# Kernel optimization log

Measured on AMD Instinct MI355X. Metric: run time of the kernel, lower is better.

## Reference

```python
import jax, jax.numpy as jnp
import numpy as np

SIZE = 256


def setup_inputs() -> dict:
    key = jax.random.key(0)
    ks = jax.random.split(key, 16)
    B, T, S, V = 16, 128, 512, 32000
    s = SIZE
    inp = {}
    inp["inputs"] = jax.random.randint(ks[0], (B, T), 0, V)
    inp["features"] = jax.random.normal(ks[1], (B, S, 2 * s), dtype=jnp.float32)
    # parameters (PyTorch-style: y = x @ W.T + b)
    inp["emb"] = jax.random.normal(ks[2], (V, s), dtype=jnp.float32)
    inp["W_ih"] = jax.random.normal(ks[3], (4 * s, 2 * s), dtype=jnp.float32) * 0.05
    inp["W_hh"] = jax.random.normal(ks[4], (4 * s, s), dtype=jnp.float32) * 0.05
    inp["b_ih"] = jax.random.normal(ks[5], (4 * s,), dtype=jnp.float32) * 0.05
    inp["b_hh"] = jax.random.normal(ks[6], (4 * s,), dtype=jnp.float32) * 0.05
    inp["Wq"] = jax.random.normal(ks[7], (s, s), dtype=jnp.float32) * 0.05
    inp["bq"] = jax.random.normal(ks[8], (s,), dtype=jnp.float32) * 0.05
    inp["Wk"] = jax.random.normal(ks[9], (s, 2 * s), dtype=jnp.float32) * 0.05
    inp["bk"] = jax.random.normal(ks[10], (s,), dtype=jnp.float32) * 0.05
    inp["Wv"] = jax.random.normal(ks[11], (s, 2 * s), dtype=jnp.float32) * 0.05
    inp["bv"] = jax.random.normal(ks[12], (s,), dtype=jnp.float32) * 0.05
    inp["Wo"] = jax.random.normal(ks[13], (V, 2 * s), dtype=jnp.float32) * 0.05
    inp["bo"] = jax.random.normal(ks[14], (V,), dtype=jnp.float32) * 0.05
    return inp


def _decode(inputs, features, emb, W_ih, W_hh, b_ih, b_hh,
            Wq, bq, Wk, bk, Wv, bv, Wo, bo):
    B, T = inputs.shape
    s = emb.shape[1]
    embeddings = emb[inputs]                      # [B, T, s]
    # features are constant across timesteps -> hoist key/value projections
    keys = features @ Wk.T + bk                   # [B, S, s]
    values = features @ Wv.T + bv                 # [B, S, s]

    def step(carry, emb_t):
        h, c, context = carry
        x = jnp.concatenate([emb_t, context], axis=1)          # [B, 2s]
        gates = x @ W_ih.T + b_ih + h @ W_hh.T + b_hh          # [B, 4s]
        i, f, g, o = jnp.split(gates, 4, axis=1)               # PyTorch gate order
        i, f, o = jax.nn.sigmoid(i), jax.nn.sigmoid(f), jax.nn.sigmoid(o)
        g = jnp.tanh(g)
        c_new = f * c + i * g
        h_new = o * jnp.tanh(c_new)
        # attention
        query = h_new @ Wq.T + bq                              # [B, s]
        scores = jnp.einsum('bsd,bd->bs', keys, query)         # [B, S]
        weights = jax.nn.softmax(scores, axis=1)
        ctx = jnp.einsum('bsd,bs->bd', values, weights)        # [B, s]
        out = jnp.concatenate([h_new, ctx], axis=1) @ Wo.T + bo  # [B, V]
        return (h_new, c_new, ctx), out

    h0 = jnp.zeros((B, s), dtype=embeddings.dtype)
    c0 = jnp.zeros((B, s), dtype=embeddings.dtype)
    ctx0 = jnp.zeros((B, s), dtype=embeddings.dtype)
    _, outs = jax.lax.scan(step, (h0, c0, ctx0), jnp.swapaxes(embeddings, 0, 1))
    return jnp.swapaxes(outs, 0, 1)               # [B, T, V]


def reference(inputs, features, emb, W_ih, W_hh, b_ih, b_hh,
              Wq, bq, Wk, bk, Wv, bv, Wo, bo):
    return _decode(inputs, features, emb, W_ih, W_hh, b_ih, b_hh,
                   Wq, bq, Wk, bk, Wv, bv, Wo, bo)
```

## Files before the change

kernel.cpp:

```cpp
#include <hip/hip_runtime.h>
#include <hip/hip_fp16.h>

#define DEVI __device__ __forceinline__

typedef __attribute__((ext_vector_type(4))) float f32x4;
typedef __attribute__((ext_vector_type(8))) short bf16x8;
typedef __attribute__((ext_vector_type(8))) _Float16 f16x8;
typedef __attribute__((ext_vector_type(2))) _Float16 f16x2;
typedef unsigned long long ull;

DEVI ushort f2bf(float x) {
  union { float f; unsigned u; } v; v.f = x;
  unsigned r = v.u + 0x7fffu + ((v.u >> 16) & 1u);
  return (ushort)(r >> 16);
}
DEVI float bf2f(ushort b) {
  union { unsigned u; float f; } v; v.u = ((unsigned)b) << 16; return v.f;
}
DEVI unsigned packh2(float a, float b) {
  return ((unsigned)__half_as_ushort(__float2half(b)) << 16) |
         (unsigned)__half_as_ushort(__float2half(a));
}
DEVI float dot2(unsigned a, unsigned b, float c) {
#if __has_builtin(__builtin_amdgcn_fdot2)
  return __builtin_amdgcn_fdot2(__builtin_bit_cast(f16x2, a),
                                __builtin_bit_cast(f16x2, b), c, false);
#else
  f16x2 ha = __builtin_bit_cast(f16x2, a), hb = __builtin_bit_cast(f16x2, b);
  return c + (float)ha[0] * (float)hb[0] + (float)ha[1] * (float)hb[1];
#endif
}
DEVI float sigmoidf_(float x) { return 1.f / (1.f + __expf(-x)); }
DEVI float tanh_fast(float x) {
  float e = __expf(2.f * x);
  return 1.f - 2.f / (e + 1.f);
}

DEVI void gstore64(ull* p, ull v) {
  __hip_atomic_store(p, v, __ATOMIC_RELAXED, __HIP_MEMORY_SCOPE_AGENT);
}
DEVI ull gload64(const ull* p) {
  return __hip_atomic_load(p, __ATOMIC_RELAXED, __HIP_MEMORY_SCOPE_AGENT);
}

template<bool SPLIT, bool ABF16, bool BBF16, bool SWZ>
__global__ __launch_bounds__(256)
void gemm_kernel(const void* __restrict__ A_, int lda, const int* __restrict__ Aidx,
                 const void* __restrict__ Bw_, int ldb,
                 const float* __restrict__ bias, float* __restrict__ C,
                 int N, int K)
{
  constexpr int BK  = SPLIT ? 32 : 64;
  constexpr int LDT = BK + 8;
  constexpr int NV  = (128 * BK / 4) / 256;

  __shared__ ushort Ah[128 * LDT];
  __shared__ ushort Bh[128 * LDT];
  __shared__ ushort Al[SPLIT ? 128 * LDT : 4];
  __shared__ ushort Bl[SPLIT ? 128 * LDT : 4];

  int bm, bn;
  if (SWZ) {
    int bid = blockIdx.x;
    int r8 = bid & 7, k = bid >> 3;
    int x = k & 15, yhi = k >> 4;
    int y = yhi * 8 + r8;
    if (y >= 250) return;
    bm = x * 128; bn = y * 128;
  } else {
    bm = blockIdx.x * 128; bn = blockIdx.y * 128;
  }

  const int tid  = threadIdx.x;
  const int lane = tid & 63, wave = tid >> 6;
  const int wr   = wave >> 1, wc = wave & 1;
  const int fr   = lane & 15, quad = lane >> 4;

  f32x4 acc[4][4] = {};

  for (int kt = 0; kt < K; kt += BK) {
    __syncthreads();
#pragma unroll
    for (int i = 0; i < NV; ++i) {
      int v   = i * 256 + tid;
      int row = v / (BK / 4);
      int c4  = (v % (BK / 4)) * 4;
      int arow = Aidx ? Aidx[bm + row] : (bm + row);
      if (ABF16) {
        const ushort* A = (const ushort*)A_;
        ushort4 h = *reinterpret_cast<const ushort4*>(A + (size_t)arow * lda + kt + c4);
        *reinterpret_cast<ushort4*>(&Ah[row * LDT + c4]) = h;
      } else {
        const float* A = (const float*)A_;
        const float4 x = *reinterpret_cast<const float4*>(A + (size_t)arow * lda + kt + c4);
        ushort4 h; h.x = f2bf(x.x); h.y = f2bf(x.y); h.z = f2bf(x.z); h.w = f2bf(x.w);
        *reinterpret_cast<ushort4*>(&Ah[row * LDT + c4]) = h;
        if (SPLIT) {
          ushort4 l;
          l.x = f2bf(x.x - bf2f(h.x)); l.y = f2bf(x.y - bf2f(h.y));
          l.z = f2bf(x.z - bf2f(h.z)); l.w = f2bf(x.w - bf2f(h.w));
          *reinterpret_cast<ushort4*>(&Al[row * LDT + c4]) = l;
        }
      }
    }
#pragma unroll
    for (int i = 0; i < NV; ++i) {
      int v   = i * 256 + tid;
      int row = v / (BK / 4);
      int c4  = (v % (BK / 4)) * 4;
      if (BBF16) {
        const ushort* B16 = (const ushort*)Bw_;
        ushort4 h = *reinterpret_cast<const ushort4*>(B16 + (size_t)(bn + row) * ldb + kt + c4);
        *reinterpret_cast<ushort4*>(&Bh[row * LDT + c4]) = h;
      } else {
        const float* Bw = (const float*)Bw_;
        const float4 x = *reinterpret_cast<const float4*>(Bw + (size_t)(bn + row) * ldb + kt + c4);
        ushort4 h; h.x = f2bf(x.x); h.y = f2bf(x.y); h.z = f2bf(x.z); h.w = f2bf(x.w);
        *reinterpret_cast<ushort4*>(&Bh[row * LDT + c4]) = h;
        if (SPLIT) {
          ushort4 l;
          l.x = f2bf(x.x - bf2f(h.x)); l.y = f2bf(x.y - bf2f(h.y));
          l.z = f2bf(x.z - bf2f(h.z)); l.w = f2bf(x.w - bf2f(h.w));
          *reinterpret_cast<ushort4*>(&Bl[row * LDT + c4]) = l;
        }
      }
    }
    __syncthreads();
#pragma unroll
    for (int ks = 0; ks < BK; ks += 32) {
      bf16x8 ah[4], bh[4];
#pragma unroll
      for (int i = 0; i < 4; ++i) {
        ah[i] = *reinterpret_cast<const bf16x8*>(&Ah[(wr * 64 + i * 16 + fr) * LDT + ks + quad * 8]);
        bh[i] = *reinterpret_cast<const bf16x8*>(&Bh[(wc * 64 + i * 16 + fr) * LDT + ks + quad * 8]);
      }
      if (SPLIT) {
        bf16x8 al[4], bl[4];
#pragma unroll
        for (int i = 0; i < 4; ++i) {
          al[i] = *reinterpret_cast<const bf16x8*>(&Al[(wr * 64 + i * 16 + fr) * LDT + ks + quad * 8]);
          bl[i] = *reinterpret_cast<const bf16x8*>(&Bl[(wc * 64 + i * 16 + fr) * LDT + ks + quad * 8]);
        }
#pragma unroll
        for (int i = 0; i < 4; ++i)
#pragma unroll
          for (int j = 0; j < 4; ++j) {
            acc[i][j] = __builtin_amdgcn_mfma_f32_16x16x32_bf16(ah[i], bh[j], acc[i][j], 0, 0, 0);
            acc[i][j] = __builtin_amdgcn_mfma_f32_16x16x32_bf16(ah[i], bl[j], acc[i][j], 0, 0, 0);
            acc[i][j] = __builtin_amdgcn_mfma_f32_16x16x32_bf16(al[i], bh[j], acc[i][j], 0, 0, 0);
          }
      } else {
#pragma unroll
        for (int i = 0; i < 4; ++i)
#pragma unroll
          for (int j = 0; j < 4; ++j)
            acc[i][j] = __builtin_amdgcn_mfma_f32_16x16x32_bf16(ah[i], bh[j], acc[i][j], 0, 0, 0);
      }
    }
  }
#pragma unroll
  for (int i = 0; i < 4; ++i)
#pragma unroll
    for (int j = 0; j < 4; ++j)
#pragma unroll
      for (int r = 0; r < 4; ++r) {
        int m = bm + wr * 64 + i * 16 + quad * 4 + r;
        int n = bn + wc * 64 + j * 16 + fr;
        float vv = acc[i][j][r];
        if (bias) vv += bias[n];
        C[(size_t)m * N + n] = vv;
      }
}

__global__ __launch_bounds__(256)
void prep2_kernel(const float* __restrict__ Wk, const float* __restrict__ Wq,
                  const float* __restrict__ Wv, const float* __restrict__ bk,
                  const float* __restrict__ bq, const float* __restrict__ b_ih,
                  const float* __restrict__ b_hh, const float* __restrict__ bv,
                  float* __restrict__ Bcomb, float* __restrict__ bias512,
                  float* __restrict__ bsum, float* __restrict__ wkbq,
                  float* __restrict__ cbbv)
{
  __shared__ float col[256];
  __shared__ float red[256];
  const int blk = blockIdx.x, tid = threadIdx.x;
  if (blk < 256) {
    const int e = blk;
    float cv = Wq[(size_t)tid * 256 + e];
    col[tid] = cv;
    red[tid] = bk[tid] * cv;
    __syncthreads();
    float a0 = 0.f, a1 = 0.f;
    for (int d = 0; d < 256; ++d) {
      float wq = col[d];
      a0 = fmaf(Wk[(size_t)d * 512 + tid], wq, a0);
      a1 = fmaf(Wk[(size_t)d * 512 + 256 + tid], wq, a1);
    }
    Bcomb[(size_t)(256 + e) * 512 + tid] = a0;
    Bcomb[(size_t)(256 + e) * 512 + 256 + tid] = a1;
    if (tid == 0) {
      float s = 0.f;
      for (int d = 0; d < 256; ++d) s += red[d];
      bias512[256 + e] = s;
    }
  } else {
    for (int i = tid; i < 256 * 512 / 4; i += 256)
      reinterpret_cast<float4*>(Bcomb)[i] = reinterpret_cast<const float4*>(Wv)[i];
    bias512[tid] = bv[tid];
    for (int i = tid; i < 1024; i += 256) bsum[i] = b_ih[i] + b_hh[i];
    float bqv = bq[tid];
    col[tid] = bqv;
    red[tid] = bk[tid] * bqv;
    __syncthreads();
    float a0 = 0.f, a1 = 0.f;
    for (int d = 0; d < 256; ++d) {
      float v = col[d];
      a0 = fmaf(Wk[(size_t)d * 512 + tid], v, a0);
      a1 = fmaf(Wk[(size_t)d * 512 + 256 + tid], v, a1);
    }
    wkbq[tid] = a0; wkbq[256 + tid] = a1;
    if (tid == 0) {
      float s = 0.f;
      for (int d = 0; d < 256; ++d) s += red[d];
      cbbv[0] = s;
    }
  }
}

__global__ void sb2_kernel(const float* __restrict__ features,
                           const float* __restrict__ wkbq,
                           const float* __restrict__ cbbv,
                           float* __restrict__ sb)
{
  int row  = blockIdx.x * 4 + (threadIdx.x >> 6);
  int lane = threadIdx.x & 63;
  const float* fr = features + (size_t)row * 512;
  float acc = 0.f;
#pragma unroll
  for (int k = 0; k < 8; ++k) acc = fmaf(fr[k * 64 + lane], wkbq[k * 64 + lane], acc);
#pragma unroll
  for (int off = 1; off < 64; off <<= 1) acc += __shfl_xor(acc, off);
  if (lane == 0) sb[row] = acc + cbbv[0];
}

__global__ void cvt_kernel(const float* __restrict__ src, ushort* __restrict__ dst, int n4)
{
  int i = blockIdx.x * 256 + threadIdx.x;
  if (i < n4) {
    float4 x = reinterpret_cast<const float4*>(src)[i];
    ushort4 h; h.x = f2bf(x.x); h.y = f2bf(x.y); h.z = f2bf(x.z); h.w = f2bf(x.w);
    reinterpret_cast<ushort4*>(dst)[i] = h;
  }
}

struct ScanSmem2 {
  unsigned k2p[64][131];
  unsigned vtp[256][35];
  unsigned xw[288];
  unsigned psp[32];
  float Erow[128];
  float gout[128];
  float ml[8][2];
  float part[8][130];
  float sc[8][64];
  float sbs[64];
};

DEVI int xwi(int w) { return (w >> 6) * 72 + (w & 63); }

__global__ __launch_bounds__(512, 1)
void scan2_kernel(const float* __restrict__ E, const float* __restrict__ KV2,
                  const float* __restrict__ sbg,
                  const float* __restrict__ W_ih, const float* __restrict__ W_hh,
                  ushort* __restrict__ hcb16,
                  ull* __restrict__ Hx,
                  ull* __restrict__ Px)
{
  extern __shared__ char smraw[];
  ScanSmem2& sm = *reinterpret_cast<ScanSmem2*>(smraw);
  const int g = blockIdx.x, tid = threadIdx.x;
  const int b = g >> 3, ss = g & 7;

  for (int idx = tid; idx < 64 * 128; idx += 512) {
    int j = idx >> 7, i = idx & 127;
    const float* src = KV2 + (size_t)(b * 512 + ss * 64 + j) * 512 + 256 + 2 * i;
    sm.k2p[j][i] = packh2(src[0], src[1]);
  }
  for (int idx = tid; idx < 256 * 32; idx += 512) {
    int e = idx >> 5, jp = idx & 31;
    float v0 = KV2[(size_t)(b * 512 + ss * 64 + 2 * jp) * 512 + e];
    float v1 = KV2[(size_t)(b * 512 + ss * 64 + 2 * jp + 1) * 512 + e];
    sm.vtp[e][jp] = packh2(v0, v1);
  }
  if (tid < 64) sm.sbs[tid] = sbg[b * 512 + ss * 64 + tid];
  for (int i = tid; i < 288; i += 512) sm.xw[i] = 0;

  const int r  = tid >> 2, h4 = tid & 3;
  const int grow = (r >> 5) * 256 + ss * 32 + (r & 31);
  const float* wsrc = (h4 < 2)
      ? (W_ih + (size_t)grow * 512 + 256 + h4 * 128)
      : (W_hh + (size_t)grow * 256 + (h4 - 2) * 128);
  unsigned wreg[64];
#pragma unroll
  for (int i = 0; i < 32; ++i) {
    float4 w4 = reinterpret_cast<const float4*>(wsrc)[i];
    wreg[2 * i]     = packh2(w4.x, w4.y);
    wreg[2 * i + 1] = packh2(w4.z, w4.w);
  }

  float c_reg = 0.f;
  __syncthreads();

  const size_t hxb = (size_t)b * 128;
  const size_t pxb = (size_t)b * (8 * 130);

  for (int t = 0; t <= 128; ++t) {
    float epf = 0.f;
    if (t < 128 && tid < 128)
      epf = E[(size_t)(b * 128 + t) * 1024 + (tid >> 5) * 256 + ss * 32 + (tid & 31)];

    float accg = 0.f;
    if (t > 0) {
      const unsigned tag = (unsigned)t;
      const ull* PxP = Px + (size_t)((t - 1) & 1) * (16 * 8 * 130) + pxb;
      const int e2 = tid & 127, q = tid >> 7;
      const ull* p1 = &PxP[(2 * q) * 130 + e2];
      const ull* p2 = &PxP[(2 * q + 1) * 130 + e2];
      ull w1 = gload64(p1), w2 = gload64(p2);
      const ull* pm = &PxP[(tid >> 1) * 130 + 128 + (tid & 1)];
      ull wm = (tid < 16) ? gload64(pm) : 0;

      if (h4 >= 2) {
        const unsigned* xsrc = sm.xw + h4 * 72;
#pragma unroll
        for (int i = 0; i < 16; ++i) {
          uint4 xv = *reinterpret_cast<const uint4*>(xsrc + 4 * i);
          accg = dot2(wreg[4 * i + 0], xv.x, accg);
          accg = dot2(wreg[4 * i + 1], xv.y, accg);
          accg = dot2(wreg[4 * i + 2], xv.z, accg);
          accg = dot2(wreg[4 * i + 3], xv.w, accg);
        }
      }

      if (tid < 16) {
        while ((unsigned)(wm >> 32) != tag) { __builtin_amdgcn_s_sleep(1); wm = gload64(pm); }
        sm.ml[tid >> 1][tid & 1] = __uint_as_float((unsigned)wm);
      }
      while ((unsigned)(w1 >> 32) != tag) { __builtin_amdgcn_s_sleep(1); w1 = gload64(p1); }
      while ((unsigned)(w2 >> 32) != tag) { __builtin_amdgcn_s_sleep(1); w2 = gload64(p2); }
      __syncthreads();
      float M = sm.ml[0][0];
#pragma unroll
      for (int s3 = 1; s3 < 8; ++s3) M = fmaxf(M, sm.ml[s3][0]);
      float L = 0.f;
#pragma unroll
      for (int s3 = 0; s3 < 8; ++s3) L += sm.ml[s3][1] * __expf(sm.ml[s3][0] - M);
      float rcpL = 1.f / L;
      float wf0 = __expf(sm.ml[2 * q][0] - M);
      float wf1 = __expf(sm.ml[2 * q + 1][0] - M);
      f16x2 x1 = __builtin_bit_cast(f16x2, (unsigned)w1);
      f16x2 x2 = __builtin_bit_cast(f16x2, (unsigned)w2);
      float2 pw0; pw0.x = wf0 * (float)x1[0] + wf1 * (float)x2[0];
      float2 pw1; pw1.x = wf0 * (float)x1[1] + wf1 * (float)x2[1];
      sm.part[2 * q][e2]     = pw0.x;
      sm.part[2 * q + 1][e2] = pw1.x;
      __syncthreads();
      {
        const int l = tid & 63;
        float2 f0[8];
#pragma unroll
        for (int s4 = 0; s4 < 8; ++s4)
          f0[s4] = *reinterpret_cast<const float2*>(&sm.part[s4][2 * l]);
        float c00 = (f0[0].x + f0[2].x + f0[4].x + f0[6].x) * rcpL;
        float c01 = (f0[1].x + f0[3].x + f0[5].x + f0[7].x) * rcpL;
        float c10 = (f0[0].y + f0[2].y + f0[4].y + f0[6].y) * rcpL;
        float c11 = (f0[1].y + f0[3].y + f0[5].y + f0[7].y) * rcpL;
        sm.xw[xwi(2 * l)]     = packh2(c00, c01);
        sm.xw[xwi(2 * l + 1)] = packh2(c10, c11);
        if (tid < 64) {
          ushort4 st;
          st.x = f2bf(c00); st.y = f2bf(c01); st.z = f2bf(c10); st.w = f2bf(c11);
          *reinterpret_cast<ushort4*>(
              hcb16 + (size_t)(b * 128 + (t - 1)) * 512 + 256 + 4 * l) = st;
        }
      }
    }
    if (t == 128) break;
    if (tid < 128) sm.Erow[tid] = epf;

    if (t > 0) {
      asm volatile("s_waitcnt lgkmcnt(0)" ::: "memory");
      __builtin_amdgcn_sched_barrier(0);
      if (h4 < 2) {
        const unsigned* xsrc = sm.xw + h4 * 72;
#pragma unroll
        for (int i = 0; i < 16; ++i) {
          uint4 xv = *reinterpret_cast<const uint4*>(xsrc + 4 * i);
          accg = dot2(wreg[4 * i + 0], xv.x, accg);
          accg = dot2(wreg[4 * i + 1], xv.y, accg);
          accg = dot2(wreg[4 * i + 2], xv.z, accg);
          accg = dot2(wreg[4 * i + 3], xv.w, accg);
        }
      }
    }
    accg += __shfl_xor(accg, 1);
    accg += __shfl_xor(accg, 2);
    if (h4 == 0) sm.gout[r] = accg;
    __syncthreads();

    if (tid < 32) {
      float gi = sm.gout[tid]      + sm.Erow[tid];
      float gf = sm.gout[32 + tid] + sm.Erow[32 + tid];
      float gg = sm.gout[64 + tid] + sm.Erow[64 + tid];
      float go = sm.gout[96 + tid] + sm.Erow[96 + tid];
      float iv = sigmoidf_(gi), fv = sigmoidf_(gf), ov = sigmoidf_(go);
      float gv = tanh_fast(gg);
      c_reg = fv * c_reg + iv * gv;
      float hn = ov * tanh_fast(c_reg);
      hcb16[(size_t)(b * 128 + t) * 512 + ss * 32 + tid] = f2bf(hn);
      float ho = __shfl_xor(hn, 1);
      if (!(tid & 1)) {
        unsigned pk = packh2(hn, ho);
        int w = ss * 16 + (tid >> 1);
        sm.xw[xwi(128 + w)] = pk;
        gstore64(&Hx[(size_t)(t & 1) * 2048 + hxb + w],
                 ((ull)(unsigned)(t + 1) << 32) | pk);
      }
    }
    if (tid < 128 && (tid >> 4) != ss) {
      const ull* hp = &Hx[(size_t)(t & 1) * 2048 + hxb + tid];
      ull w = gload64(hp);
      while ((unsigned)(w >> 32) != (unsigned)(t + 1)) {
        __builtin_amdgcn_s_sleep(1); w = gload64(hp);
      }
      sm.xw[xwi(128 + tid)] = (unsigned)w;
    }
    __syncthreads();

    {
      const int j = tid & 63, qq = tid >> 6;
      float acc2 = 0.f;
#pragma unroll
      for (int i = 0; i < 16; ++i)
        acc2 = dot2(sm.k2p[j][qq * 16 + i], sm.xw[xwi(128 + qq * 16 + i)], acc2);
      sm.sc[qq][j] = acc2;
    }
    __syncthreads();
    if (tid < 64) {
      float s = sm.sc[0][tid] + sm.sc[1][tid] + sm.sc[2][tid] + sm.sc[3][tid]
              + sm.sc[4][tid] + sm.sc[5][tid] + sm.sc[6][tid] + sm.sc[7][tid]
              + sm.sbs[tid];
      float mx = s;
#pragma unroll
      for (int off = 1; off < 64; off <<= 1) mx = fmaxf(mx, __shfl_xor(mx, off));
      float p = __expf(s - mx);
      float ls = p;
#pragma unroll
      for (int off = 1; off < 64; off <<= 1) ls += __shfl_xor(ls, off);
      if (tid == 0) {
        ull tg = (ull)(unsigned)(t + 1) << 32;
        ull* PxS = Px + (size_t)(t & 1) * (16 * 8 * 130) + pxb + ss * 130;
        gstore64(&PxS[128], tg | __float_as_uint(mx));
        gstore64(&PxS[129], tg | __float_as_uint(ls));
      }
      float ph = __shfl_xor(p, 1);
      if (!(tid & 1)) sm.psp[tid >> 1] = packh2(p, ph);
    }
    __syncthreads();
    if (tid < 256) {
      float acc2 = 0.f;
#pragma unroll
      for (int jp = 0; jp < 32; ++jp) acc2 = dot2(sm.psp[jp], sm.vtp[tid][jp], acc2);
      float ao = __shfl_xor(acc2, 1);
      if (!(tid & 1)) {
        ull* PxS = Px + (size_t)(t & 1) * (16 * 8 * 130) + pxb + ss * 130;
        gstore64(&PxS[tid >> 1], ((ull)(unsigned)(t + 1) << 32) | packh2(acc2, ao));
      }
    }
  }
}

extern "C" void kernel_launch(void* const* d_in, const int* in_sizes, int n_in,
                              void* d_out, int out_size, void* d_ws, size_t ws_size,
                              hipStream_t stream)
{
  const int*   inputs   = (const int*)  d_in[0];
  const float* features = (const float*)d_in[1];
  const float* emb      = (const float*)d_in[2];
  const float* W_ih     = (const float*)d_in[3];
  const float* W_hh     = (const float*)d_in[4];
  const float* b_ih     = (const float*)d_in[5];
  const float* b_hh     = (const float*)d_in[6];
  const float* Wq       = (const float*)d_in[7];
  const float* bq       = (const float*)d_in[8];
  const float* Wk       = (const float*)d_in[9];
  const float* bk       = (const float*)d_in[10];
  const float* Wv       = (const float*)d_in[11];
  const float* bv       = (const float*)d_in[12];
  const float* Wo       = (const float*)d_in[13];
  const float* bo       = (const float*)d_in[14];
  float* out = (float*)d_out;

  char* ws = (char*)d_ws;
  size_t off = 0;
  auto alloc = [&](size_t bytes) -> char* {
    char* p = ws + off;
    off += (bytes + 255) & ~size_t(255);
    return p;
  };
  float*  KV2   = (float*) alloc((size_t)8192 * 512 * 4);
  float*  E     = (float*) alloc((size_t)2048 * 1024 * 4);
  float*  Bcomb = (float*) alloc((size_t)512 * 512 * 4);
  float*  bias512 = (float*)alloc((size_t)512 * 4);
  float*  sb    = (float*) alloc((size_t)8192 * 4);
  float*  bsum  = (float*) alloc((size_t)1024 * 4);
  float*  wkbq  = (float*) alloc((size_t)512 * 4);
  float*  cbbv  = (float*) alloc((size_t)64 * 4);
  ushort* hcb16 = (ushort*)alloc((size_t)2048 * 512 * 2);
  ull*    Hx    = (ull*)   alloc((size_t)2 * 16 * 128 * 8);
  ull*    Px    = (ull*)   alloc((size_t)2 * 16 * 8 * 130 * 8);

  const size_t woBytes = (size_t)32000 * 512 * 2;
  ushort* Wo16 = nullptr;
  if (off + woBytes + 256 <= ws_size) Wo16 = (ushort*)alloc(woBytes);

  hipMemsetAsync(Hx, 0, (size_t)2 * 16 * 128 * 8, stream);
  hipMemsetAsync(Px, 0, (size_t)2 * 16 * 8 * 130 * 8, stream);

  prep2_kernel<<<257, 256, 0, stream>>>(Wk, Wq, Wv, bk, bq, b_ih, b_hh, bv,
                                        Bcomb, bias512, bsum, wkbq, cbbv);

  gemm_kernel<true, false, false, false><<<dim3(64, 4), 256, 0, stream>>>(
      features, 512, nullptr, Bcomb, 512, bias512, KV2, 512, 512);
  sb2_kernel<<<2048, 256, 0, stream>>>(features, wkbq, cbbv, sb);
  gemm_kernel<true, false, false, false><<<dim3(16, 8), 256, 0, stream>>>(
      emb, 256, inputs, W_ih, 512, bsum, E, 1024, 256);

  if (Wo16) cvt_kernel<<<16000, 256, 0, stream>>>(Wo, Wo16, 32000 * 512 / 4);

  hipFuncSetAttribute(reinterpret_cast<const void*>(scan2_kernel),
                      hipFuncAttributeMaxDynamicSharedMemorySize, (int)sizeof(ScanSmem2));
  scan2_kernel<<<128, 512, sizeof(ScanSmem2), stream>>>(E, KV2, sb, W_ih, W_hh,
                                                        hcb16, Hx, Px);

  if (Wo16)
    gemm_kernel<false, true, true, true><<<4096, 256, 0, stream>>>(
        hcb16, 512, nullptr, Wo16, 512, bo, out, 32000, 512);
  else
    gemm_kernel<false, true, false, true><<<4096, 256, 0, stream>>>(
        hcb16, 512, nullptr, Wo, 512, bo, out, 32000, 512);
}
```

Before: 1.427 ms.

## Add direct-to-LDS bf16 output GEMM and simplify context reduction in scan

Adds a dedicated output-projection GEMM that moves bf16 tiles from global memory straight into LDS with global_load_lds, with BK=32 and an unpadded LDS layout, instead of staging them through registers. The swizzled block mapping moves into this new kernel, and the generic GEMM loses its SWZ template parameter. In the scan kernel, the context partial reduction is rearranged into a [4][128][2] layout that 128 threads each sum, and an explicit syncthreads replaces the manual waitcnt/sched_barrier before the gate dot products. The unpadded LDS layout may cause bank conflicts on the fragment reads, and the extra barrier adds per-step synchronisation to the serial scan.

```diff
diff --git a/kernel.cpp b/kernel.cpp
--- a/kernel.cpp
+++ b/kernel.cpp
@@ -43,7 +43,13 @@
   return __hip_atomic_load(p, __ATOMIC_RELAXED, __HIP_MEMORY_SCOPE_AGENT);
 }
 
-template<bool SPLIT, bool ABF16, bool BBF16, bool SWZ>
+DEVI void gload_lds16(const ushort* g, ushort* l) {
+  __builtin_amdgcn_global_load_lds(
+      (const __attribute__((address_space(1))) void*)g,
+      (__attribute__((address_space(3))) void*)l, 16, 0, 0);
+}
+
+template<bool SPLIT, bool ABF16, bool BBF16>
 __global__ __launch_bounds__(256)
 void gemm_kernel(const void* __restrict__ A_, int lda, const int* __restrict__ Aidx,
                  const void* __restrict__ Bw_, int ldb,
@@ -59,19 +65,8 @@
   __shared__ ushort Al[SPLIT ? 128 * LDT : 4];
   __shared__ ushort Bl[SPLIT ? 128 * LDT : 4];
 
-  int bm, bn;
-  if (SWZ) {
-    int bid = blockIdx.x;
-    int r8 = bid & 7, k = bid >> 3;
-    int x = k & 15, yhi = k >> 4;
-    int y = yhi * 8 + r8;
-    if (y >= 250) return;
-    bm = x * 128; bn = y * 128;
-  } else {
-    bm = blockIdx.x * 128; bn = blockIdx.y * 128;
-  }
-
   const int tid  = threadIdx.x;
+  const int bm   = blockIdx.x * 128, bn = blockIdx.y * 128;
   const int lane = tid & 63, wave = tid >> 6;
   const int wr   = wave >> 1, wc = wave & 1;
   const int fr   = lane & 15, quad = lane >> 4;
@@ -173,6 +168,69 @@
 }
 
 __global__ __launch_bounds__(256)
+void ogemm_kernel(const ushort* __restrict__ A, const ushort* __restrict__ B,
+                  const float* __restrict__ bias, float* __restrict__ C,
+                  int N, int K)
+{
+  __shared__ ushort Ah[128 * 32];
+  __shared__ ushort Bh[128 * 32];
+
+  const int bid = blockIdx.x;
+  const int r8 = bid & 7, k2 = bid >> 3;
+  const int bx = k2 & 15, yhi = k2 >> 4;
+  const int by = yhi * 8 + r8;
+  if (by >= 250) return;
+  const int bm = bx * 128, bn = by * 128;
+
+  const int tid  = threadIdx.x;
+  const int lane = tid & 63, w = tid >> 6;
+  const int wr   = w >> 1, wc = w & 1;
+  const int fr   = lane & 15, quad = lane >> 4;
+
+  const int srow = w * 16 + (lane >> 2);
+  const int scol = (lane & 3) * 8;
+  const ushort* ga = A + (size_t)(bm + srow) * K + scol;
+  const ushort* gb = B + (size_t)(bn + srow) * K + scol;
+  ushort* da = Ah + w * 512;
+  ushort* db = Bh + w * 512;
+  const size_t half = (size_t)64 * K;
+
+  f32x4 acc[4][4] = {};
+
+  for (int kt = 0; kt < K; kt += 32) {
+    __syncthreads();
+    gload_lds16(ga + kt, da);
+    gload_lds16(ga + kt + half, da + 2048);
+    gload_lds16(gb + kt, db);
+    gload_lds16(gb + kt + half, db + 2048);
+    __syncthreads();
+
+    bf16x8 ah[4], bh[4];
+#pragma unroll
+    for (int i = 0; i < 4; ++i) {
+      ah[i] = *reinterpret_cast<const bf16x8*>(&Ah[(wr * 64 + i * 16 + fr) * 32 + quad * 8]);
+      bh[i] = *reinterpret_cast<const bf16x8*>(&Bh[(wc * 64 + i * 16 + fr) * 32 + quad * 8]);
+    }
+#pragma unroll
+    for (int i = 0; i < 4; ++i)
+#pragma unroll
+      for (int j = 0; j < 4; ++j)
+        acc[i][j] = __builtin_amdgcn_mfma_f32_16x16x32_bf16(ah[i], bh[j], acc[i][j], 0, 0, 0);
+  }
+
+#pragma unroll
+  for (int i = 0; i < 4; ++i)
+#pragma unroll
+    for (int j = 0; j < 4; ++j)
+#pragma unroll
+      for (int r = 0; r < 4; ++r) {
+        int m = bm + wr * 64 + i * 16 + quad * 4 + r;
+        int n = bn + wc * 64 + j * 16 + fr;
+        C[(size_t)m * N + n] = acc[i][j][r] + bias[n];
+      }
+}
+
+__global__ __launch_bounds__(256)
 void prep2_kernel(const float* __restrict__ Wk, const float* __restrict__ Wq,
                   const float* __restrict__ Wv, const float* __restrict__ bk,
                   const float* __restrict__ bq, const float* __restrict__ b_ih,
@@ -261,7 +319,7 @@
   float Erow[128];
   float gout[128];
   float ml[8][2];
-  float part[8][130];
+  float cpart[4][128][2];
   float sc[8][64];
   float sbs[64];
 };
@@ -360,47 +418,32 @@
       float wf1 = __expf(sm.ml[2 * q + 1][0] - M);
       f16x2 x1 = __builtin_bit_cast(f16x2, (unsigned)w1);
       f16x2 x2 = __builtin_bit_cast(f16x2, (unsigned)w2);
-      float2 pw0; pw0.x = wf0 * (float)x1[0] + wf1 * (float)x2[0];
-      float2 pw1; pw1.x = wf0 * (float)x1[1] + wf1 * (float)x2[1];
-      sm.part[2 * q][e2]     = pw0.x;
-      sm.part[2 * q + 1][e2] = pw1.x;
+      sm.cpart[q][e2][0] = wf0 * (float)x1[0] + wf1 * (float)x2[0];
+      sm.cpart[q][e2][1] = wf0 * (float)x1[1] + wf1 * (float)x2[1];
       __syncthreads();
-      {
-        const int l = tid & 63;
-        float2 f0[8];
-#pragma unroll
-        for (int s4 = 0; s4 < 8; ++s4)
-          f0[s4] = *reinterpret_cast<const float2*>(&sm.part[s4][2 * l]);
-        float c00 = (f0[0].x + f0[2].x + f0[4].x + f0[6].x) * rcpL;
-        float c01 = (f0[1].x + f0[3].x + f0[5].x + f0[7].x) * rcpL;
-        float c10 = (f0[0].y + f0[2].y + f0[4].y + f0[6].y) * rcpL;
-        float c11 = (f0[1].y + f0[3].y + f0[5].y + f0[7].y) * rcpL;
-        sm.xw[xwi(2 * l)]     = packh2(c00, c01);
-        sm.xw[xwi(2 * l + 1)] = packh2(c10, c11);
-        if (tid < 64) {
-          ushort4 st;
-          st.x = f2bf(c00); st.y = f2bf(c01); st.z = f2bf(c10); st.w = f2bf(c11);
-          *reinterpret_cast<ushort4*>(
-              hcb16 + (size_t)(b * 128 + (t - 1)) * 512 + 256 + 4 * l) = st;
-        }
+      if (tid < 128) {
+        float c0 = (sm.cpart[0][tid][0] + sm.cpart[1][tid][0]
+                  + sm.cpart[2][tid][0] + sm.cpart[3][tid][0]) * rcpL;
+        float c1 = (sm.cpart[0][tid][1] + sm.cpart[1][tid][1]
+                  + sm.cpart[2][tid][1] + sm.cpart[3][tid][1]) * rcpL;
+        sm.xw[xwi(tid)] = packh2(c0, c1);
+        ushort* dst = hcb16 + (size_t)(b * 128 + (t - 1)) * 512 + 256 + 2 * tid;
+        dst[0] = f2bf(c0); dst[1] = f2bf(c1);
       }
     }
     if (t == 128) break;
     if (tid < 128) sm.Erow[tid] = epf;
-
-    if (t > 0) {
-      asm volatile("s_waitcnt lgkmcnt(0)" ::: "memory");
-      __builtin_amdgcn_sched_barrier(0);
-      if (h4 < 2) {
-        const unsigned* xsrc = sm.xw + h4 * 72;
-#pragma unroll
-        for (int i = 0; i < 16; ++i) {
-          uint4 xv = *reinterpret_cast<const uint4*>(xsrc + 4 * i);
-          accg = dot2(wreg[4 * i + 0], xv.x, accg);
-          accg = dot2(wreg[4 * i + 1], xv.y, accg);
-          accg = dot2(wreg[4 * i + 2], xv.z, accg);
-          accg = dot2(wreg[4 * i + 3], xv.w, accg);
-        }
+    __syncthreads();
+
+    if (t > 0 && h4 < 2) {
+      const unsigned* xsrc = sm.xw + h4 * 72;
+#pragma unroll
+      for (int i = 0; i < 16; ++i) {
+        uint4 xv = *reinterpret_cast<const uint4*>(xsrc + 4 * i);
+        accg = dot2(wreg[4 * i + 0], xv.x, accg);
+        accg = dot2(wreg[4 * i + 1], xv.y, accg);
+        accg = dot2(wreg[4 * i + 2], xv.z, accg);
+        accg = dot2(wreg[4 * i + 3], xv.w, accg);
       }
     }
     accg += __shfl_xor(accg, 1);
@@ -530,10 +573,10 @@
   prep2_kernel<<<257, 256, 0, stream>>>(Wk, Wq, Wv, bk, bq, b_ih, b_hh, bv,
                                         Bcomb, bias512, bsum, wkbq, cbbv);
 
-  gemm_kernel<true, false, false, false><<<dim3(64, 4), 256, 0, stream>>>(
+  gemm_kernel<true, false, false><<<dim3(64, 4), 256, 0, stream>>>(
       features, 512, nullptr, Bcomb, 512, bias512, KV2, 512, 512);
   sb2_kernel<<<2048, 256, 0, stream>>>(features, wkbq, cbbv, sb);
-  gemm_kernel<true, false, false, false><<<dim3(16, 8), 256, 0, stream>>>(
+  gemm_kernel<true, false, false><<<dim3(16, 8), 256, 0, stream>>>(
       emb, 256, inputs, W_ih, 512, bsum, E, 1024, 256);
 
   if (Wo16) cvt_kernel<<<16000, 256, 0, stream>>>(Wo, Wo16, 32000 * 512 / 4);
@@ -544,9 +587,8 @@
                                                         hcb16, Hx, Px);
 
   if (Wo16)
-    gemm_kernel<false, true, true, true><<<4096, 256, 0, stream>>>(
-        hcb16, 512, nullptr, Wo16, 512, bo, out, 32000, 512);
+    ogemm_kernel<<<4096, 256, 0, stream>>>(hcb16, Wo16, bo, out, 32000, 512);
   else
-    gemm_kernel<false, true, false, true><<<4096, 256, 0, stream>>>(
+    gemm_kernel<false, true, false><<<dim3(16, 250), 256, 0, stream>>>(
         hcb16, 512, nullptr, Wo, 512, bo, out, 32000, 512);
 }
```

Result: faster. 1.246 ms (-12.7%).
